# Performance work log

Hardware: AMD Instinct MI355X
Metric: run time of the kernel (lower is better)

The kernel has to match this reference:

```python
import jax, jax.numpy as jnp
import numpy as np

TINY = np.finfo(np.float32).tiny


def setup_inputs() -> dict:
    key = jax.random.key(0)
    k1, k2, k3 = jax.random.split(key, 3)
    B, IN, OUT = 4096, 4096, 1024
    x = jax.random.normal(k1, (B, IN), dtype=jnp.float32)
    weight = jax.random.normal(k2, (IN, OUT), dtype=jnp.float32)
    uniform = jax.random.uniform(k3, (IN, OUT), dtype=jnp.float32)
    T = jnp.ones((1,), dtype=jnp.float32)
    return {"x": x, "weight": weight, "uniform": uniform, "T": T}


def reference(x, weight, uniform, T):
    # training-path forward of ConcreteLayer
    # uniform -> (1 - tiny) * u + tiny, then Gumbel noise
    u = (1.0 - TINY) * uniform + TINY
    gumbel = -jnp.log(-jnp.log(u))                      # [in, out]
    noisy_logits = (weight + gumbel) / T                # temperature scaling
    samples = jax.nn.softmax(noisy_logits, axis=1)      # softmax over out dim (torch default for 2D)
    out = jnp.einsum('bi,ik->bk', x, samples)           # [batch, out]
    return out
```

## Files before the change

### kernel.cpp

```cpp
#include <hip/hip_runtime.h>
#include <cstdint>
#include <cstddef>


#define TINYF 1.17549435082228750797e-38f
#define LN2F 0.69314718055994530942f
#define LOG2EF 1.44269504088896340736f

typedef unsigned short u16;
typedef __attribute__((ext_vector_type(8))) short bf16x8;
typedef __attribute__((ext_vector_type(4))) float f32x4;

__device__ __forceinline__ u16 f2bf(float f) {
  union { float f; uint32_t u; } v; v.f = f;
  uint32_t r = v.u + 0x7FFFu + ((v.u >> 16) & 1u);
  return (u16)(r >> 16);
}

__device__ __forceinline__ float log2_hw(float x) { return __builtin_amdgcn_logf(x); }
__device__ __forceinline__ float exp2_hw(float x) { return __builtin_amdgcn_exp2f(x); }

__device__ __forceinline__ float gumbel_fast(float u) {
  float t = -log2_hw(u);
  return -LN2F * log2_hw(t * LN2F);
}
__device__ __forceinline__ float exp_fast(float x) { return exp2_hw(x * LOG2EF); }

__device__ __forceinline__ void gld_lds16(const void* g, void* l) {
  __builtin_amdgcn_global_load_lds(
      (__attribute__((address_space(1))) void*)(g),
      (__attribute__((address_space(3))) void*)(l), 16, 0, 0);
}

__global__ void trans_exp_kernel(const float* __restrict__ W, const float* __restrict__ U,
                                 const float* __restrict__ Tp, u16* __restrict__ BT,
                                 float* __restrict__ d) {
  __shared__ float tile[64][65];
  const int k0 = blockIdx.x * 64, n0 = blockIdx.y * 64;
  const int t = threadIdx.x;
  const float invT = 1.0f / Tp[0];
  {
    const int nn4 = (t & 15) * 4, kq = t >> 4;
#pragma unroll
    for (int r = 0; r < 4; ++r) {
      int kk = r * 16 + kq;
      size_t gi = (size_t)(k0 + kk) * 1024 + (n0 + nn4);
      float4 w = *(const float4*)&W[gi];
      float4 u = *(const float4*)&U[gi];
      float e0 = exp_fast((w.x + gumbel_fast(u.x * (1.0f - TINYF) + TINYF)) * invT);
      float e1 = exp_fast((w.y + gumbel_fast(u.y * (1.0f - TINYF) + TINYF)) * invT);
      float e2 = exp_fast((w.z + gumbel_fast(u.z * (1.0f - TINYF) + TINYF)) * invT);
      float e3 = exp_fast((w.w + gumbel_fast(u.w * (1.0f - TINYF) + TINYF)) * invT);
      tile[kk][nn4 + 0] = e0; tile[kk][nn4 + 1] = e1;
      tile[kk][nn4 + 2] = e2; tile[kk][nn4 + 3] = e3;
      float s = (e0 + e1) + (e2 + e3);
#pragma unroll
      for (int m = 8; m > 0; m >>= 1) s += __shfl_xor(s, m, 16);
      if ((t & 15) == 0) atomicAdd(&d[k0 + kk], s);
    }
  }
  __syncthreads();
  {
    const int kk4 = (t & 15) * 4, nq = t >> 4;
#pragma unroll
    for (int r = 0; r < 4; ++r) {
      int nn = r * 16 + nq;
      ushort4 o;
      o.x = f2bf(tile[kk4 + 0][nn]);
      o.y = f2bf(tile[kk4 + 1][nn]);
      o.z = f2bf(tile[kk4 + 2][nn]);
      o.w = f2bf(tile[kk4 + 3][nn]);
      *(ushort4*)&BT[(size_t)(n0 + nn) * 4096 + (k0 + kk4)] = o;
    }
  }
}

__global__ void cast_zero_kernel(const float4* __restrict__ x, const float4* __restrict__ d4,
                                 ushort4* __restrict__ xb, float4* __restrict__ out,
                                 int n4x, int n4o) {
  int i = blockIdx.x * blockDim.x + threadIdx.x;
  if (i < n4x) {
    int col4 = i & 1023;
    float4 v = x[i];
    float4 dd = d4[col4];
    ushort4 o;
    o.x = f2bf(v.x / dd.x); o.y = f2bf(v.y / dd.y);
    o.z = f2bf(v.z / dd.z); o.w = f2bf(v.w / dd.w);
    xb[i] = o;
  } else {
    int j = i - n4x;
    if (j < n4o) out[j] = make_float4(0.f, 0.f, 0.f, 0.f);
  }
}

#define TM 128
#define TN 128
#define TK 64
#define SPLITK 4

__launch_bounds__(256)
__global__ void gemm_bt_kernel(const u16* __restrict__ A, const u16* __restrict__ BT,
                               float* __restrict__ C, int M, int N, int K) {
  __shared__ u16 As[TM * TK];
  __shared__ u16 Bs[TN * TK];

  const int tid = threadIdx.x;
  const int lane = tid & 63, w = tid >> 6;
  const int wm = w >> 1, wn = w & 1;
  const int m0 = blockIdx.x * TM, n0 = blockIdx.y * TN;
  const int quad = lane >> 4, r16 = lane & 15;
  const int srow = lane >> 3;
  const int sg = (lane & 7) ^ srow;

  const int kz = blockIdx.z;
  const int Kh = K / SPLITK;
  const u16* Ak = A + (size_t)kz * Kh;
  const u16* Bk = BT + (size_t)kz * Kh;

  f32x4 acc[4][4] = {};

  for (int kt = 0; kt < Kh; kt += TK) {
    __syncthreads();
#pragma unroll
    for (int c = 0; c < 4; ++c) {
      int chunk = w * 4 + c;
      gld_lds16(Ak + (size_t)(m0 + chunk * 8 + srow) * K + kt + sg * 8, (char*)As + chunk * 1024);
      gld_lds16(Bk + (size_t)(n0 + chunk * 8 + srow) * K + kt + sg * 8, (char*)Bs + chunk * 1024);
    }
    __syncthreads();

#pragma unroll
    for (int ss = 0; ss < 2; ++ss) {
      bf16x8 aF[4], bF[4];
#pragma unroll
      for (int mi = 0; mi < 4; ++mi) {
        int row = wm * 64 + mi * 16 + r16;
        aF[mi] = *(const bf16x8*)((const char*)As + row * 128 + (((ss * 4 + quad) ^ (row & 7)) * 16));
      }
#pragma unroll
      for (int ni = 0; ni < 4; ++ni) {
        int row = wn * 64 + ni * 16 + r16;
        bF[ni] = *(const bf16x8*)((const char*)Bs + row * 128 + (((ss * 4 + quad) ^ (row & 7)) * 16));
      }
#pragma unroll
      for (int mi = 0; mi < 4; ++mi)
#pragma unroll
        for (int ni = 0; ni < 4; ++ni)
          acc[mi][ni] = __builtin_amdgcn_mfma_f32_16x16x32_bf16(aF[mi], bF[ni], acc[mi][ni], 0, 0, 0);
    }
  }

#pragma unroll
  for (int mi = 0; mi < 4; ++mi)
#pragma unroll
    for (int ni = 0; ni < 4; ++ni)
#pragma unroll
      for (int r = 0; r < 4; ++r) {
        int row = m0 + wm * 64 + mi * 16 + quad * 4 + r;
        int col = n0 + wn * 64 + ni * 16 + r16;
        atomicAdd(&C[(size_t)row * N + col], acc[mi][ni][r]);
      }
}

extern "C" void kernel_launch(void* const* d_in, const int* in_sizes, int n_in,
                              void* d_out, int out_size, void* d_ws, size_t ws_size,
                              hipStream_t stream) {
  const int M = 4096, K = 4096, N = 1024;
  const float* x = (const float*)d_in[0];
  const float* W = (const float*)d_in[1];
  const float* U = (const float*)d_in[2];
  const float* Tp = (const float*)d_in[3];
  float* out = (float*)d_out;

  char* ws = (char*)d_ws;
  u16* xb = (u16*)ws;
  u16* bt = (u16*)(ws + (size_t)M * K * 2);
  float* dsum = (float*)(ws + (size_t)M * K * 2 + (size_t)N * K * 2);

  hipMemsetAsync(dsum, 0, K * sizeof(float), stream);
  trans_exp_kernel<<<dim3(K / 64, N / 64), 256, 0, stream>>>(W, U, Tp, bt, dsum);
  const int n4x = M * K / 4, n4o = M * N / 4;
  cast_zero_kernel<<<dim3((n4x + n4o) / 256), 256, 0, stream>>>(
      (const float4*)x, (const float4*)dsum, (ushort4*)xb, (float4*)out, n4x, n4o);
  gemm_bt_kernel<<<dim3(M / TM, N / TN, SPLITK), 256, 0, stream>>>(xb, bt, out, M, N, K);
}
```

Before: 217.1 us.

## Double-buffer LDS tiles in GEMM and halve split-K factor

The GEMM now uses two LDS buffers for A and B, issuing the async global-to-LDS loads for the next K tile before computing on the current one, with one barrier per tile instead of two. Split-K drops from 4 to 2, which halves the fp32 atomicAdd traffic to the output but also halves the grid to 512 blocks with longer K loops. LDS use per block doubles to 64 KB, which may reduce occupancy. The loop assumes an even tile count per split (Kh/TK = 32 here).

```diff
diff --git a/kernel.cpp b/kernel.cpp
--- a/kernel.cpp
+++ b/kernel.cpp
@@ -96,13 +96,13 @@
 #define TM 128
 #define TN 128
 #define TK 64
-#define SPLITK 4
+#define SPLITK 2
 
 __launch_bounds__(256)
 __global__ void gemm_bt_kernel(const u16* __restrict__ A, const u16* __restrict__ BT,
                                float* __restrict__ C, int M, int N, int K) {
-  __shared__ u16 As[TM * TK];
-  __shared__ u16 Bs[TN * TK];
+  __shared__ u16 As[2][TM * TK];
+  __shared__ u16 Bs[2][TN * TK];
 
   const int tid = threadIdx.x;
   const int lane = tid & 63, w = tid >> 6;
@@ -119,36 +119,56 @@
 
   f32x4 acc[4][4] = {};
 
-  for (int kt = 0; kt < Kh; kt += TK) {
+#define STAGE(buf, kt)                                                                   \
+  {                                                                                      \
+    _Pragma("unroll") for (int c = 0; c < 4; ++c) {                                      \
+      int chunk = w * 4 + c;                        \
+      gld_lds16(Ak + (size_t)(m0 + chunk * 8 + srow) * K + (kt) + sg * 8,                \
+                (char*)&As[buf][0] + chunk * 1024);                                      \
+      gld_lds16(Bk + (size_t)(n0 + chunk * 8 + srow) * K + (kt) + sg * 8,                \
+                (char*)&Bs[buf][0] + chunk * 1024);                                      \
+    }                                                                                    \
+  }
+
+#define COMPUTE(buf)                                                                     \
+  {                                                                                      \
+    _Pragma("unroll") for (int ss = 0; ss < 2; ++ss) {                                   \
+      bf16x8 aF[4], bF[4];                                                               \
+      _Pragma("unroll") for (int mi = 0; mi < 4; ++mi) {                                 \
+        int row = wm * 64 + mi * 16 + r16;                                               \
+        aF[mi] = *(const bf16x8*)((const char*)&As[buf][0] + row * 128 +                 \
+                                  (((ss * 4 + quad) ^ (row & 7)) * 16));                 \
+      }                                                                                  \
+      _Pragma("unroll") for (int ni = 0; ni < 4; ++ni) {                                 \
+        int row = wn * 64 + ni * 16 + r16;                                               \
+        bF[ni] = *(const bf16x8*)((const char*)&Bs[buf][0] + row * 128 +                 \
+                                  (((ss * 4 + quad) ^ (row & 7)) * 16));                 \
+      }                                                                                  \
+      _Pragma("unroll") for (int mi = 0; mi < 4; ++mi)                                   \
+          _Pragma("unroll") for (int ni = 0; ni < 4; ++ni)                               \
+              acc[mi][ni] =                                                              \
+          __builtin_amdgcn_mfma_f32_16x16x32_bf16(aF[mi], bF[ni], acc[mi][ni], 0, 0, 0); \
+    }                                                                                    \
+  }
+
+  STAGE(0, 0)
+  __syncthreads();
+  const int nt = Kh / TK;
+  for (int t = 0; t < nt - 2; t += 2) {
+    STAGE(1, (t + 1) * TK)
+    COMPUTE(0)
     __syncthreads();
-#pragma unroll
-    for (int c = 0; c < 4; ++c) {
-      int chunk = w * 4 + c;
-      gld_lds16(Ak + (size_t)(m0 + chunk * 8 + srow) * K + kt + sg * 8, (char*)As + chunk * 1024);
-      gld_lds16(Bk + (size_t)(n0 + chunk * 8 + srow) * K + kt + sg * 8, (char*)Bs + chunk * 1024);
-    }
+    STAGE(0, (t + 2) * TK)
+    COMPUTE(1)
     __syncthreads();
-
-#pragma unroll
-    for (int ss = 0; ss < 2; ++ss) {
-      bf16x8 aF[4], bF[4];
-#pragma unroll
-      for (int mi = 0; mi < 4; ++mi) {
-        int row = wm * 64 + mi * 16 + r16;
-        aF[mi] = *(const bf16x8*)((const char*)As + row * 128 + (((ss * 4 + quad) ^ (row & 7)) * 16));
-      }
-#pragma unroll
-      for (int ni = 0; ni < 4; ++ni) {
-        int row = wn * 64 + ni * 16 + r16;
-        bF[ni] = *(const bf16x8*)((const char*)Bs + row * 128 + (((ss * 4 + quad) ^ (row & 7)) * 16));
-      }
-#pragma unroll
-      for (int mi = 0; mi < 4; ++mi)
-#pragma unroll
-        for (int ni = 0; ni < 4; ++ni)
-          acc[mi][ni] = __builtin_amdgcn_mfma_f32_16x16x32_bf16(aF[mi], bF[ni], acc[mi][ni], 0, 0, 0);
-    }
-  }
+  }
+  STAGE(1, (nt - 1) * TK)
+  COMPUTE(0)
+  __syncthreads();
+  COMPUTE(1)
+
+#undef STAGE
+#undef COMPUTE
 
 #pragma unroll
   for (int mi = 0; mi < 4; ++mi)
```

Result: faster. 196.4 us (-9.5%).
